# Kernel tuning notes

Measured on AMD Instinct MI355X. Metric: run time of the kernel, lower is better.

## Reference

```python
import jax, jax.numpy as jnp
import numpy as np

B, H, S, D = 4, 16, 2048, 64

def setup_inputs() -> dict:
    key = jax.random.key(0)
    kq, kk, kv = jax.random.split(key, 3)
    q = jax.random.normal(kq, (B, H, S, D), dtype=jnp.float32)
    k = jax.random.normal(kk, (B, H, S, D), dtype=jnp.float32)
    v = jax.random.normal(kv, (B, H, S, D), dtype=jnp.float32)
    return {"q": q, "k": k, "v": v}

def reference(q, k, v):
    # dots: [b,h,i,j] = q . k (NO 1/sqrt(d) scaling, matching source)
    dots = jnp.einsum('bhid,bhjd->bhij', q, k)
    # causal=False (and the source's causal mask is a no-op bug anyway)
    attn = jax.nn.softmax(dots, axis=-1)
    # out: [b,h,i,d] = sum_j attn[b,h,i,j] * v[b,h,j,d]
    return jnp.einsum('bhjd,bhij->bhid', v, attn)
```

## Files before the change

kernel.cpp:

```cpp
#include <hip/hip_runtime.h>
#include <hip/hip_bf16.h>
#include <stdint.h>

#define B_ 4
#define H_ 16
#define S_ 2048
#define D_ 64
#define QBLK 128
#define KBLK 64
#define LDW 72
#define LOG2E 1.44269504088896340736f

typedef __attribute__((ext_vector_type(8))) short short8;
typedef __attribute__((ext_vector_type(4))) float f32x4;
typedef __attribute__((ext_vector_type(16))) float f32x16;
typedef _Float16 f16x8 __attribute__((ext_vector_type(8)));
typedef _Float16 f16x4 __attribute__((ext_vector_type(4)));
typedef __fp16 fp16x2 __attribute__((ext_vector_type(2)));

__device__ __forceinline__ unsigned short f2bf(float f) {
  union { float f; unsigned int u; } x; x.f = f;
  unsigned int u = x.u;
  unsigned int r = (u + 0x7FFFu + ((u >> 16) & 1u)) >> 16;
  return (unsigned short)r;
}
__device__ __forceinline__ float bf2f(unsigned short h) {
  union { unsigned int u; float f; } y; y.u = ((unsigned int)h) << 16;
  return y.f;
}

__device__ __forceinline__ unsigned pkrtz(float a, float b) {
  union { fp16x2 h; unsigned u; } c;
  c.h = __builtin_amdgcn_cvt_pkrtz(a, b);
  return c.u;
}
__device__ __forceinline__ fp16x2 u2h(unsigned u) {
  union { unsigned u; fp16x2 h; } c; c.u = u; return c.h;
}

__device__ __forceinline__ float fast_exp2(float x) {
#if __has_builtin(__builtin_amdgcn_exp2f)
  return __builtin_amdgcn_exp2f(x);
#else
  return exp2f(x);
#endif
}

__device__ __forceinline__ void swap32(unsigned &a, unsigned &b) {
#if __has_builtin(__builtin_amdgcn_permlane32_swap)
  typedef int i32x2 __attribute__((ext_vector_type(2)));
  i32x2 r = __builtin_amdgcn_permlane32_swap((int)a, (int)b, false, false);
  a = (unsigned)r[0]; b = (unsigned)r[1];
#else
  asm("v_permlane32_swap_b32 %0, %1" : "+v"(a), "+v"(b));
#endif
}

__device__ __forceinline__ float pairmax(float x) {
  unsigned a = __float_as_uint(x), b = a;
  swap32(a, b);
  return fmaxf(__uint_as_float(a), __uint_as_float(b));
}
__device__ __forceinline__ float pairsum(float x) {
  unsigned a = __float_as_uint(x), b = a;
  swap32(a, b);
  return __uint_as_float(a) + __uint_as_float(b);
}

#define GLOAD16(g, l) __builtin_amdgcn_global_load_lds( \
    (const __attribute__((address_space(1))) unsigned int*)(g), \
    (__attribute__((address_space(3))) unsigned int*)(l), 16, 0, 0)

__global__ void prep_k(const float* __restrict__ K, _Float16* __restrict__ Kp) {
  int e4 = (blockIdx.x * 256 + threadIdx.x) * 4;
  int bh  = e4 >> 17;
  int rem = e4 & 131071;
  int s   = rem >> 6;
  int d0  = rem & 63;
  const float4 kv = *(const float4*)(K + (size_t)e4);
  f16x4 h;
  h[0] = (_Float16)kv.x; h[1] = (_Float16)kv.y;
  h[2] = (_Float16)kv.z; h[3] = (_Float16)kv.w;
  size_t off = ((size_t)bh * S_ + s) * 128 + (unsigned)((d0 * 2) ^ ((s & 7) << 4));
  *(f16x4*)((char*)Kp + off) = h;
}

__global__ void prep_v(const float* __restrict__ V, _Float16* __restrict__ Vt) {
  __shared__ _Float16 tile[64][66];
  int bh = blockIdx.x >> 5;
  int st = blockIdx.x & 31;
  const float* Vb = V + ((size_t)bh * S_ + st * 64) * 64;
  int tid = threadIdx.x;
  #pragma unroll
  for (int i = 0; i < 4; ++i) {
    int idx = i * 1024 + tid * 4;
    int r = idx >> 6, c = idx & 63;
    float4 vv = *(const float4*)(Vb + (size_t)r * 64 + c);
    f16x4 o;
    o[0] = (_Float16)vv.x; o[1] = (_Float16)vv.y;
    o[2] = (_Float16)vv.z; o[3] = (_Float16)vv.w;
    *(f16x4*)&tile[r][c] = o;
  }
  __syncthreads();
  int chunk = tid & 15;
  int dbase = tid >> 4;
  size_t outb = (size_t)bh * (64 * S_ * 2) + (size_t)st * 128;
  #pragma unroll
  for (int i = 0; i < 4; ++i) {
    int d = dbase + i * 16;
    f16x4 o;
    o[0] = tile[chunk * 4 + 0][d];
    o[1] = tile[chunk * 4 + 1][d];
    o[2] = tile[chunk * 4 + 2][d];
    o[3] = tile[chunk * 4 + 3][d];
    size_t off = outb + (size_t)d * (S_ * 2) + (unsigned)((chunk * 8) ^ ((d & 7) << 4));
    *(f16x4*)((char*)Vt + off) = o;
  }
}

__global__ __launch_bounds__(256)
void attn_fwd8(const float* __restrict__ Q, const _Float16* __restrict__ Kg,
               const _Float16* __restrict__ Vg, float* __restrict__ O) {
  __shared__ char smem[32768];

  const int tid  = threadIdx.x;
  const int lane = tid & 63;
  const int wid  = tid >> 6;
  const int l31  = lane & 31;
  const int hi   = lane >> 5;

  const int bh    = blockIdx.x;
  const int qtile = blockIdx.y;

  const char* KB = (const char*)Kg + (size_t)bh * (S_ * 128);
  const char* VB = (const char*)Vg + (size_t)bh * (64 * S_ * 2);
  const float* Qb = Q + (size_t)bh * S_ * D_;
  float*       Ob = O + (size_t)bh * S_ * D_;

  const int qrow = qtile * QBLK + wid * 32 + l31;
  f16x8 qf[4];
  #pragma unroll
  for (int ds = 0; ds < 4; ++ds) {
    const float* qp = Qb + (size_t)qrow * D_ + ds * 16 + hi * 8;
    float4 a = *(const float4*)(qp);
    float4 b = *(const float4*)(qp + 4);
    qf[ds][0] = (_Float16)(a.x * LOG2E); qf[ds][1] = (_Float16)(a.y * LOG2E);
    qf[ds][2] = (_Float16)(a.z * LOG2E); qf[ds][3] = (_Float16)(a.w * LOG2E);
    qf[ds][4] = (_Float16)(b.x * LOG2E); qf[ds][5] = (_Float16)(b.y * LOG2E);
    qf[ds][6] = (_Float16)(b.z * LOG2E); qf[ds][7] = (_Float16)(b.w * LOG2E);
  }

  f32x16 oacc[2];
  #pragma unroll
  for (int dn = 0; dn < 2; ++dn)
    #pragma unroll
    for (int r = 0; r < 16; ++r) oacc[dn][r] = 0.f;
  float m_r = -INFINITY, l_r = 0.f;

  f32x16 zero16;
  #pragma unroll
  for (int r = 0; r < 16; ++r) zero16[r] = 0.f;

  #define STAGE(buf, kb)                                                        \
    {                                                                           \
      char* Kl_ = smem + (buf) * 16384;                                         \
      char* Vl_ = Kl_ + 8192;                                                   \
      _Pragma("unroll")                                                         \
      for (int c = 0; c < 4; ++c) {                                             \
        int id = c * 4 + wid;                                                   \
        if (id < 8) {                                                           \
          GLOAD16(KB + (size_t)(kb) * 128 + id * 1024 + lane * 16,              \
                  Kl_ + id * 1024);                                             \
        } else {                                                                \
          int i = id - 8;                                                       \
          GLOAD16(VB + (size_t)(i * 8 + (lane >> 3)) * (S_ * 2)                 \
                     + ((kb) >> 6) * 128 + (lane & 7) * 16,                     \
                  Vl_ + i * 1024);                                              \
        }                                                                       \
      }                                                                         \
    }

  STAGE(0, 0);
  __syncthreads();

  for (int it = 0; it < S_ / KBLK; ++it) {
    const int cur = it & 1;
    if (it < S_ / KBLK - 1) STAGE(cur ^ 1, (it + 1) * KBLK);

    const char* Kl = smem + cur * 16384;
    const char* Vl = Kl + 8192;

    f32x16 sacc_a, sacc_b;
    __builtin_amdgcn_s_setprio(1);
    {
      const int row = l31;
      const int sw = (row & 7) << 4;
      sacc_a = __builtin_amdgcn_mfma_f32_32x32x16_f16(
          *(const f16x8*)(Kl + row * 128 + ((0 * 32 + hi * 16) ^ sw)), qf[0], zero16, 0, 0, 0);
      #pragma unroll
      for (int ds = 1; ds < 4; ++ds)
        sacc_a = __builtin_amdgcn_mfma_f32_32x32x16_f16(
            *(const f16x8*)(Kl + row * 128 + ((ds * 32 + hi * 16) ^ sw)), qf[ds], sacc_a, 0, 0, 0);
    }
    {
      const int row = 32 + l31;
      const int sw = (row & 7) << 4;
      sacc_b = __builtin_amdgcn_mfma_f32_32x32x16_f16(
          *(const f16x8*)(Kl + row * 128 + ((0 * 32 + hi * 16) ^ sw)), qf[0], zero16, 0, 0, 0);
      #pragma unroll
      for (int ds = 1; ds < 4; ++ds)
        sacc_b = __builtin_amdgcn_mfma_f32_32x32x16_f16(
            *(const f16x8*)(Kl + row * 128 + ((ds * 32 + hi * 16) ^ sw)), qf[ds], sacc_b, 0, 0, 0);
    }
    __builtin_amdgcn_s_setprio(0);

    {
      float v0 = fmaxf(fmaxf(sacc_a[0], sacc_a[1]), sacc_a[2]);
      float v1 = fmaxf(fmaxf(sacc_a[3], sacc_a[4]), sacc_a[5]);
      float v2 = fmaxf(fmaxf(sacc_a[6], sacc_a[7]), sacc_a[8]);
      float v3 = fmaxf(fmaxf(sacc_a[9], sacc_a[10]), sacc_a[11]);
      float v4 = fmaxf(fmaxf(sacc_a[12], sacc_a[13]), sacc_a[14]);
      float w0 = fmaxf(fmaxf(v0, v1), v2);
      float w1 = fmaxf(fmaxf(v3, v4), sacc_a[15]);
      float mx = pairmax(fmaxf(w0, w1));
      if (!__all(mx <= m_r + 8.f)) {
        float nm = fmaxf(m_r, mx);
        float sc = fast_exp2(m_r - nm);
        m_r = nm; l_r *= sc;
        #pragma unroll
        for (int dn = 0; dn < 2; ++dn)
          #pragma unroll
          for (int r = 0; r < 16; ++r) oacc[dn][r] *= sc;
      }
      unsigned ww[8];
      #pragma unroll
      for (int r1 = 0; r1 < 4; ++r1) {
        float p0 = fast_exp2(sacc_a[4 * r1 + 0] - m_r);
        float p1 = fast_exp2(sacc_a[4 * r1 + 1] - m_r);
        float p2 = fast_exp2(sacc_a[4 * r1 + 2] - m_r);
        float p3 = fast_exp2(sacc_a[4 * r1 + 3] - m_r);
        ww[r1 * 2 + 0] = pkrtz(p0, p1);
        ww[r1 * 2 + 1] = pkrtz(p2, p3);
      }
      {
        const fp16x2 ones = {(__fp16)1.f, (__fp16)1.f};
        float rA = __builtin_amdgcn_fdot2(u2h(ww[0]), ones, 0.f, false);
        float rB = __builtin_amdgcn_fdot2(u2h(ww[1]), ones, 0.f, false);
        rA = __builtin_amdgcn_fdot2(u2h(ww[2]), ones, rA, false);
        rB = __builtin_amdgcn_fdot2(u2h(ww[3]), ones, rB, false);
        rA = __builtin_amdgcn_fdot2(u2h(ww[4]), ones, rA, false);
        rB = __builtin_amdgcn_fdot2(u2h(ww[5]), ones, rB, false);
        rA = __builtin_amdgcn_fdot2(u2h(ww[6]), ones, rA, false);
        rB = __builtin_amdgcn_fdot2(u2h(ww[7]), ones, rB, false);
        l_r += rA + rB;
      }
      f16x8 pb0, pb1;
      {
        unsigned u0 = ww[0], u1 = ww[1], u2 = ww[2], u3 = ww[3];
        swap32(u0, u2); swap32(u1, u3);
        union { unsigned u[4]; f16x8 v; } c;
        c.u[0] = u0; c.u[1] = u1; c.u[2] = u2; c.u[3] = u3;
        pb0 = c.v;
      }
      {
        unsigned u0 = ww[4], u1 = ww[5], u2 = ww[6], u3 = ww[7];
        swap32(u0, u2); swap32(u1, u3);
        union { unsigned u[4]; f16x8 v; } c;
        c.u[0] = u0; c.u[1] = u1; c.u[2] = u2; c.u[3] = u3;
        pb1 = c.v;
      }
      __builtin_amdgcn_s_setprio(1);
      #pragma unroll
      for (int dn = 0; dn < 2; ++dn) {
        const int d = dn * 32 + l31;
        const int sw = (d & 7) << 4;
        f16x8 vf0 = *(const f16x8*)(Vl + d * 128 + ((0 * 32 + hi * 16) ^ sw));
        f16x8 vf1 = *(const f16x8*)(Vl + d * 128 + ((1 * 32 + hi * 16) ^ sw));
        oacc[dn] = __builtin_amdgcn_mfma_f32_32x32x16_f16(vf0, pb0, oacc[dn], 0, 0, 0);
        oacc[dn] = __builtin_amdgcn_mfma_f32_32x32x16_f16(vf1, pb1, oacc[dn], 0, 0, 0);
      }
      __builtin_amdgcn_s_setprio(0);
    }

    {
      float v0 = fmaxf(fmaxf(sacc_b[0], sacc_b[1]), sacc_b[2]);
      float v1 = fmaxf(fmaxf(sacc_b[3], sacc_b[4]), sacc_b[5]);
      float v2 = fmaxf(fmaxf(sacc_b[6], sacc_b[7]), sacc_b[8]);
      float v3 = fmaxf(fmaxf(sacc_b[9], sacc_b[10]), sacc_b[11]);
      float v4 = fmaxf(fmaxf(sacc_b[12], sacc_b[13]), sacc_b[14]);
      float w0 = fmaxf(fmaxf(v0, v1), v2);
      float w1 = fmaxf(fmaxf(v3, v4), sacc_b[15]);
      float mx = pairmax(fmaxf(w0, w1));
      if (!__all(mx <= m_r + 8.f)) {
        float nm = fmaxf(m_r, mx);
        float sc = fast_exp2(m_r - nm);
        m_r = nm; l_r *= sc;
        #pragma unroll
        for (int dn = 0; dn < 2; ++dn)
          #pragma unroll
          for (int r = 0; r < 16; ++r) oacc[dn][r] *= sc;
      }
      unsigned ww[8];
      #pragma unroll
      for (int r1 = 0; r1 < 4; ++r1) {
        float p0 = fast_exp2(sacc_b[4 * r1 + 0] - m_r);
        float p1 = fast_exp2(sacc_b[4 * r1 + 1] - m_r);
        float p2 = fast_exp2(sacc_b[4 * r1 + 2] - m_r);
        float p3 = fast_exp2(sacc_b[4 * r1 + 3] - m_r);
        ww[r1 * 2 + 0] = pkrtz(p0, p1);
        ww[r1 * 2 + 1] = pkrtz(p2, p3);
      }
      {
        const fp16x2 ones = {(__fp16)1.f, (__fp16)1.f};
        float rA = __builtin_amdgcn_fdot2(u2h(ww[0]), ones, 0.f, false);
        float rB = __builtin_amdgcn_fdot2(u2h(ww[1]), ones, 0.f, false);
        rA = __builtin_amdgcn_fdot2(u2h(ww[2]), ones, rA, false);
        rB = __builtin_amdgcn_fdot2(u2h(ww[3]), ones, rB, false);
        rA = __builtin_amdgcn_fdot2(u2h(ww[4]), ones, rA, false);
        rB = __builtin_amdgcn_fdot2(u2h(ww[5]), ones, rB, false);
        rA = __builtin_amdgcn_fdot2(u2h(ww[6]), ones, rA, false);
        rB = __builtin_amdgcn_fdot2(u2h(ww[7]), ones, rB, false);
        l_r += rA + rB;
      }
      f16x8 pb2, pb3;
      {
        unsigned u0 = ww[0], u1 = ww[1], u2 = ww[2], u3 = ww[3];
        swap32(u0, u2); swap32(u1, u3);
        union { unsigned u[4]; f16x8 v; } c;
        c.u[0] = u0; c.u[1] = u1; c.u[2] = u2; c.u[3] = u3;
        pb2 = c.v;
      }
      {
        unsigned u0 = ww[4], u1 = ww[5], u2 = ww[6], u3 = ww[7];
        swap32(u0, u2); swap32(u1, u3);
        union { unsigned u[4]; f16x8 v; } c;
        c.u[0] = u0; c.u[1] = u1; c.u[2] = u2; c.u[3] = u3;
        pb3 = c.v;
      }
      __builtin_amdgcn_s_setprio(1);
      #pragma unroll
      for (int dn = 0; dn < 2; ++dn) {
        const int d = dn * 32 + l31;
        const int sw = (d & 7) << 4;
        f16x8 vf2 = *(const f16x8*)(Vl + d * 128 + ((2 * 32 + hi * 16) ^ sw));
        f16x8 vf3 = *(const f16x8*)(Vl + d * 128 + ((3 * 32 + hi * 16) ^ sw));
        oacc[dn] = __builtin_amdgcn_mfma_f32_32x32x16_f16(vf2, pb2, oacc[dn], 0, 0, 0);
        oacc[dn] = __builtin_amdgcn_mfma_f32_32x32x16_f16(vf3, pb3, oacc[dn], 0, 0, 0);
      }
      __builtin_amdgcn_s_setprio(0);
    }

    __syncthreads();
  }
  #undef STAGE

  const float inv = 1.0f / pairsum(l_r);
  float* Ep = (float*)(smem + wid * 8192);
  #pragma unroll
  for (int dn = 0; dn < 2; ++dn)
    #pragma unroll
    for (int r = 0; r < 16; ++r) {
      int d = dn * 32 + (r & 3) + 8 * (r >> 2) + 4 * hi;
      Ep[d * 32 + l31] = oacc[dn][r] * inv;
    }
  __syncthreads();
  const int q2 = lane >> 1, dh = lane & 1;
  float* orow = Ob + (size_t)(qtile * QBLK + wid * 32 + q2) * D_ + dh * 32;
  #pragma unroll
  for (int c = 0; c < 8; ++c) {
    float4 o4;
    o4.x = Ep[(dh * 32 + c * 4 + 0) * 32 + q2];
    o4.y = Ep[(dh * 32 + c * 4 + 1) * 32 + q2];
    o4.z = Ep[(dh * 32 + c * 4 + 2) * 32 + q2];
    o4.w = Ep[(dh * 32 + c * 4 + 3) * 32 + q2];
    *(float4*)(orow + c * 4) = o4;
  }
}

__global__ __launch_bounds__(256, 2)
void attn_fwd(const float* __restrict__ Q, const float* __restrict__ K,
              const float* __restrict__ V, float* __restrict__ O) {
  __shared__ alignas(16) unsigned short Kh_lds[KBLK * LDW];
  __shared__ alignas(16) unsigned short Kl_lds[KBLK * LDW];
  __shared__ alignas(16) unsigned short Vt_lds[D_ * LDW];
  __shared__ alignas(16) unsigned short P_lds[4][16 * LDW];

  const int tid  = threadIdx.x;
  const int lane = tid & 63;
  const int wid  = tid >> 6;
  const int l15  = lane & 15;
  const int dgrp = lane >> 4;

  const int qtile = blockIdx.x;
  const int bh    = blockIdx.y;

  const size_t base = (size_t)bh * S_ * D_;
  const float* Qb = Q + base;
  const float* Kb = K + base;
  const float* Vb = V + base;
  float*       Ob = O + base;

  const int qrow = qtile * 64 + wid * 16 + l15;
  short8 qfh[2], qfl[2];
  {
    const float* qp = Qb + (size_t)qrow * D_ + dgrp * 8;
    #pragma unroll
    for (int s = 0; s < 2; ++s)
      #pragma unroll
      for (int j = 0; j < 8; ++j) {
        float f = qp[s * 32 + j];
        unsigned short h = f2bf(f);
        qfh[s][j] = (short)h;
        qfl[s][j] = (short)f2bf(f - bf2f(h));
      }
  }

  f32x4 oacc[4];
  #pragma unroll
  for (int t = 0; t < 4; ++t) oacc[t] = f32x4{0.f, 0.f, 0.f, 0.f};
  float m_r[4], l_r[4];
  #pragma unroll
  for (int j = 0; j < 4; ++j) { m_r[j] = -INFINITY; l_r[j] = 0.f; }

  for (int kb = 0; kb < S_; kb += KBLK) {
    __syncthreads();
    #pragma unroll
    for (int c = 0; c < 4; ++c) {
      int e = (c * 256 + tid) * 4;
      int r = e >> 6, col = e & 63;
      const float4 kv = *(const float4*)(Kb + (size_t)(kb + r) * D_ + col);
      ushort4 kh, kl;
      kh.x = f2bf(kv.x); kl.x = f2bf(kv.x - bf2f(kh.x));
      kh.y = f2bf(kv.y); kl.y = f2bf(kv.y - bf2f(kh.y));
      kh.z = f2bf(kv.z); kl.z = f2bf(kv.z - bf2f(kh.z));
      kh.w = f2bf(kv.w); kl.w = f2bf(kv.w - bf2f(kh.w));
      *(ushort4*)&Kh_lds[r * LDW + col] = kh;
      *(ushort4*)&Kl_lds[r * LDW + col] = kl;
      const float4 vv = *(const float4*)(Vb + (size_t)(kb + r) * D_ + col);
      Vt_lds[(col + 0) * LDW + r] = f2bf(vv.x);
      Vt_lds[(col + 1) * LDW + r] = f2bf(vv.y);
      Vt_lds[(col + 2) * LDW + r] = f2bf(vv.z);
      Vt_lds[(col + 3) * LDW + r] = f2bf(vv.w);
    }
    __syncthreads();

    f32x4 sa[4];
    #pragma unroll
    for (int t = 0; t < 4; ++t) {
      sa[t] = f32x4{0.f, 0.f, 0.f, 0.f};
      #pragma unroll
      for (int s = 0; s < 2; ++s) {
        const int off = (t * 16 + l15) * LDW + s * 32 + dgrp * 8;
        short8 kfh = *(const short8*)&Kh_lds[off];
        short8 kfl = *(const short8*)&Kl_lds[off];
        sa[t] = __builtin_amdgcn_mfma_f32_16x16x32_bf16(qfh[s], kfh, sa[t], 0, 0, 0);
        sa[t] = __builtin_amdgcn_mfma_f32_16x16x32_bf16(qfh[s], kfl, sa[t], 0, 0, 0);
        sa[t] = __builtin_amdgcn_mfma_f32_16x16x32_bf16(qfl[s], kfh, sa[t], 0, 0, 0);
      }
    }

    float pmax[4];
    #pragma unroll
    for (int j = 0; j < 4; ++j) {
      float mx = fmaxf(fmaxf(sa[0][j], sa[1][j]), fmaxf(sa[2][j], sa[3][j]));
      #pragma unroll
      for (int m = 1; m < 16; m <<= 1) mx = fmaxf(mx, __shfl_xor(mx, m));
      pmax[j] = mx;
    }
    float scale[4];
    #pragma unroll
    for (int j = 0; j < 4; ++j) {
      float nm = fmaxf(m_r[j], pmax[j]);
      scale[j] = __expf(m_r[j] - nm);
      m_r[j] = nm;
    }
    float rs[4] = {0.f, 0.f, 0.f, 0.f};
    #pragma unroll
    for (int t = 0; t < 4; ++t)
      #pragma unroll
      for (int j = 0; j < 4; ++j) {
        float p = __expf(sa[t][j] - m_r[j]);
        rs[j] += p;
        P_lds[wid][(dgrp * 4 + j) * LDW + t * 16 + l15] = f2bf(p);
      }
    #pragma unroll
    for (int j = 0; j < 4; ++j) {
      #pragma unroll
      for (int m = 1; m < 16; m <<= 1) rs[j] += __shfl_xor(rs[j], m);
      l_r[j] = l_r[j] * scale[j] + rs[j];
      #pragma unroll
      for (int t = 0; t < 4; ++t) oacc[t][j] *= scale[j];
    }

    #pragma unroll
    for (int s = 0; s < 2; ++s) {
      short8 pf = *(const short8*)&P_lds[wid][l15 * LDW + s * 32 + dgrp * 8];
      #pragma unroll
      for (int t = 0; t < 4; ++t) {
        short8 vf = *(const short8*)&Vt_lds[(t * 16 + l15) * LDW + s * 32 + dgrp * 8];
        oacc[t] = __builtin_amdgcn_mfma_f32_16x16x32_bf16(pf, vf, oacc[t], 0, 0, 0);
      }
    }
  }

  #pragma unroll
  for (int j = 0; j < 4; ++j) {
    float inv = 1.0f / l_r[j];
    int row = qtile * 64 + wid * 16 + dgrp * 4 + j;
    float* op = Ob + (size_t)row * D_ + l15;
    #pragma unroll
    for (int t = 0; t < 4; ++t)
      op[t * 16] = oacc[t][j] * inv;
  }
}

extern "C" void kernel_launch(void* const* d_in, const int* in_sizes, int n_in,
                              void* d_out, int out_size, void* d_ws, size_t ws_size,
                              hipStream_t stream) {
  const float* q = (const float*)d_in[0];
  const float* k = (const float*)d_in[1];
  const float* v = (const float*)d_in[2];
  float* o = (float*)d_out;
  const size_t PLANE = (size_t)B_ * H_ * S_ * 128;
  if (ws_size >= 2 * PLANE) {
    _Float16* Kp = (_Float16*)d_ws;
    _Float16* Vt = (_Float16*)((char*)d_ws + PLANE);
    prep_k<<<8192, 256, 0, stream>>>(k, Kp);
    prep_v<<<2048, 256, 0, stream>>>(v, Vt);
    attn_fwd8<<<dim3(B_ * H_, S_ / QBLK), 256, 0, stream>>>(q, Kp, Vt, o);
  } else {
    attn_fwd<<<dim3(S_ / 64, B_ * H_), 256, 0, stream>>>(q, k, v, o);
  }
}
```

Measured before the change: 142.5 us.

## Split KV range across two blocks and merge partials with combine kernel

Adds a templated attention kernel that splits the key/value sequence into NKS chunks via a third grid dimension. Each chunk writes unnormalized partial outputs plus running max and sum to workspace, and a separate combine kernel rescales and merges them. The aim is more blocks and more parallelism per CU, at the cost of extra global memory traffic for the partials and an additional kernel launch. The path is only taken when the workspace is large enough.

```diff
diff --git a/kernel.cpp b/kernel.cpp
--- a/kernel.cpp
+++ b/kernel.cpp
@@ -8,6 +8,7 @@
 #define D_ 64
 #define QBLK 128
 #define KBLK 64
+#define NT (S_ / KBLK)
 #define LDW 72
 #define LOG2E 1.44269504088896340736f
 
@@ -118,9 +119,11 @@
   }
 }
 
+template<int NKS>
 __global__ __launch_bounds__(256)
-void attn_fwd8(const float* __restrict__ Q, const _Float16* __restrict__ Kg,
-               const _Float16* __restrict__ Vg, float* __restrict__ O) {
+void attn_fwd12(const float* __restrict__ Q, const _Float16* __restrict__ Kg,
+                const _Float16* __restrict__ Vg, float* __restrict__ O,
+                float* __restrict__ Opart, float* __restrict__ ML) {
   __shared__ char smem[32768];
 
   const int tid  = threadIdx.x;
@@ -131,11 +134,13 @@
 
   const int bh    = blockIdx.x;
   const int qtile = blockIdx.y;
+  const int ks    = blockIdx.z;
+  const int t0    = ks * (NT / NKS);
+  const int t1    = t0 + (NT / NKS);
 
   const char* KB = (const char*)Kg + (size_t)bh * (S_ * 128);
   const char* VB = (const char*)Vg + (size_t)bh * (64 * S_ * 2);
   const float* Qb = Q + (size_t)bh * S_ * D_;
-  float*       Ob = O + (size_t)bh * S_ * D_;
 
   const int qrow = qtile * QBLK + wid * 32 + l31;
   f16x8 qf[4];
@@ -180,12 +185,12 @@
       }                                                                         \
     }
 
-  STAGE(0, 0);
+  STAGE(0, t0 * KBLK);
   __syncthreads();
 
-  for (int it = 0; it < S_ / KBLK; ++it) {
-    const int cur = it & 1;
-    if (it < S_ / KBLK - 1) STAGE(cur ^ 1, (it + 1) * KBLK);
+  for (int it = t0; it < t1; ++it) {
+    const int cur = (it - t0) & 1;
+    if (it < t1 - 1) STAGE(cur ^ 1, (it + 1) * KBLK);
 
     const char* Kl = smem + cur * 16384;
     const char* Vl = Kl + 8192;
@@ -354,27 +359,80 @@
   }
   #undef STAGE
 
-  const float inv = 1.0f / pairsum(l_r);
+  const float l_full = pairsum(l_r);
   float* Ep = (float*)(smem + wid * 8192);
-  #pragma unroll
-  for (int dn = 0; dn < 2; ++dn)
-    #pragma unroll
-    for (int r = 0; r < 16; ++r) {
-      int d = dn * 32 + (r & 3) + 8 * (r >> 2) + 4 * hi;
-      Ep[d * 32 + l31] = oacc[dn][r] * inv;
-    }
-  __syncthreads();
-  const int q2 = lane >> 1, dh = lane & 1;
-  float* orow = Ob + (size_t)(qtile * QBLK + wid * 32 + q2) * D_ + dh * 32;
-  #pragma unroll
-  for (int c = 0; c < 8; ++c) {
-    float4 o4;
-    o4.x = Ep[(dh * 32 + c * 4 + 0) * 32 + q2];
-    o4.y = Ep[(dh * 32 + c * 4 + 1) * 32 + q2];
-    o4.z = Ep[(dh * 32 + c * 4 + 2) * 32 + q2];
-    o4.w = Ep[(dh * 32 + c * 4 + 3) * 32 + q2];
-    *(float4*)(orow + c * 4) = o4;
-  }
+
+  if (NKS == 1) {
+    const float inv = 1.0f / l_full;
+    #pragma unroll
+    for (int dn = 0; dn < 2; ++dn)
+      #pragma unroll
+      for (int r = 0; r < 16; ++r) {
+        int d = dn * 32 + (r & 3) + 8 * (r >> 2) + 4 * hi;
+        Ep[d * 32 + l31] = oacc[dn][r] * inv;
+      }
+    __syncthreads();
+    const int q2 = lane >> 1, dh = lane & 1;
+    float* orow = O + (size_t)bh * S_ * D_
+                + (size_t)(qtile * QBLK + wid * 32 + q2) * D_ + dh * 32;
+    #pragma unroll
+    for (int c = 0; c < 8; ++c) {
+      float4 o4;
+      o4.x = Ep[(dh * 32 + c * 4 + 0) * 32 + q2];
+      o4.y = Ep[(dh * 32 + c * 4 + 1) * 32 + q2];
+      o4.z = Ep[(dh * 32 + c * 4 + 2) * 32 + q2];
+      o4.w = Ep[(dh * 32 + c * 4 + 3) * 32 + q2];
+      *(float4*)(orow + c * 4) = o4;
+    }
+  } else {
+    #pragma unroll
+    for (int dn = 0; dn < 2; ++dn)
+      #pragma unroll
+      for (int r = 0; r < 16; ++r) {
+        int d = dn * 32 + (r & 3) + 8 * (r >> 2) + 4 * hi;
+        Ep[d * 32 + l31] = oacc[dn][r];
+      }
+    if (hi == 0) {
+      size_t mli = ((size_t)ks * 64 + bh) * S_ + (qtile * QBLK + wid * 32 + l31);
+      ((float2*)ML)[mli] = make_float2(m_r, l_full);
+    }
+    __syncthreads();
+    const int q2 = lane >> 1, dh = lane & 1;
+    float* orow = Opart + (((size_t)ks * 64 + bh) * S_
+                + (qtile * QBLK + wid * 32 + q2)) * D_ + dh * 32;
+    #pragma unroll
+    for (int c = 0; c < 8; ++c) {
+      float4 o4;
+      o4.x = Ep[(dh * 32 + c * 4 + 0) * 32 + q2];
+      o4.y = Ep[(dh * 32 + c * 4 + 1) * 32 + q2];
+      o4.z = Ep[(dh * 32 + c * 4 + 2) * 32 + q2];
+      o4.w = Ep[(dh * 32 + c * 4 + 3) * 32 + q2];
+      *(float4*)(orow + c * 4) = o4;
+    }
+  }
+}
+
+__global__ void combine2(const float* __restrict__ Opart, const float* __restrict__ ML,
+                         float* __restrict__ O) {
+  const size_t NQ = (size_t)64 * S_;
+  size_t idx = (size_t)blockIdx.x * 256 + threadIdx.x;
+  size_t e4 = idx * 4;
+  size_t bhq = e4 >> 6;
+  int d0 = (int)(e4 & 63);
+  float2 ml0 = ((const float2*)ML)[bhq];
+  float2 ml1 = ((const float2*)ML)[bhq + NQ];
+  float m = fmaxf(ml0.x, ml1.x);
+  float w0 = fast_exp2(ml0.x - m);
+  float w1 = fast_exp2(ml1.x - m);
+  float inv = 1.0f / (ml0.y * w0 + ml1.y * w1);
+  float4 a = *(const float4*)(Opart + bhq * 64 + d0);
+  float4 b = *(const float4*)(Opart + (bhq + NQ) * 64 + d0);
+  float4 o;
+  o.x = (a.x * w0 + b.x * w1) * inv;
+  o.y = (a.y * w0 + b.y * w1) * inv;
+  o.z = (a.z * w0 + b.z * w1) * inv;
+  o.w = (a.w * w0 + b.w * w1) * inv;
+  *(float4*)(O + bhq * 64 + d0) = o;
 }
 
 __global__ __launch_bounds__(256, 2)
@@ -522,12 +580,23 @@
   const float* v = (const float*)d_in[2];
   float* o = (float*)d_out;
   const size_t PLANE = (size_t)B_ * H_ * S_ * 128;
-  if (ws_size >= 2 * PLANE) {
+  const size_t OPART = (size_t)2 * 64 * S_ * D_ * 4;
+  const size_t MLSZ  = (size_t)2 * 64 * S_ * 2 * 4;
+  if (ws_size >= 2 * PLANE + OPART + MLSZ) {
+    _Float16* Kp = (_Float16*)d_ws;
+    _Float16* Vt = (_Float16*)((char*)d_ws + PLANE);
+    float* Opart = (float*)((char*)d_ws + 2 * PLANE);
+    float* ML    = (float*)((char*)d_ws + 2 * PLANE + OPART);
+    prep_k<<<8192, 256, 0, stream>>>(k, Kp);
+    prep_v<<<2048, 256, 0, stream>>>(v, Vt);
+    attn_fwd12<2><<<dim3(B_ * H_, S_ / QBLK, 2), 256, 0, stream>>>(q, Kp, Vt, o, Opart, ML);
+    combine2<<<(B_ * H_ * S_ * D_) / (256 * 4), 256, 0, stream>>>(Opart, ML, o);
+  } else if (ws_size >= 2 * PLANE) {
     _Float16* Kp = (_Float16*)d_ws;
     _Float16* Vt = (_Float16*)((char*)d_ws + PLANE);
     prep_k<<<8192, 256, 0, stream>>>(k, Kp);
     prep_v<<<2048, 256, 0, stream>>>(v, Vt);
-    attn_fwd8<<<dim3(B_ * H_, S_ / QBLK), 256, 0, stream>>>(q, Kp, Vt, o);
+    attn_fwd12<1><<<dim3(B_ * H_, S_ / QBLK, 1), 256, 0, stream>>>(q, Kp, Vt, o, nullptr, nullptr);
   } else {
     attn_fwd<<<dim3(S_ / 64, B_ * H_), 256, 0, stream>>>(q, k, v, o);
   }
```

Result: slower. 167.0 us (+17.2%).
